# Kernel optimization log

Hardware: AMD Instinct MI355X
Metric: run time of the kernel (lower is better)

## Reference

```python
import jax, jax.numpy as jnp
import numpy as np

TOP_K = 2

def moe_linear(x, router_w, experts_w):
    # x: [T, din]; router_w: [din, E]; experts_w: [E, din, dout]
    T = x.shape[0]
    E = experts_w.shape[0]
    probs = jax.nn.softmax(x @ router_w, axis=-1)            # [T, E]
    topv, topi = jax.lax.top_k(probs, TOP_K)                 # [T, k]
    topv = topv / jnp.sum(topv, axis=-1, keepdims=True)      # renormalize over selected experts
    w = jnp.zeros((T, E), x.dtype).at[jnp.arange(T)[:, None], topi].set(topv)  # dense routing weights
    y = jnp.zeros((T, experts_w.shape[2]), x.dtype)
    for e in range(E):  # small fixed expert loop; avoids [T,E,dout] intermediate
        y = y + w[:, e:e+1] * (x @ experts_w[e])
    return y

def setup_inputs() -> dict:
    key = jax.random.key(0)
    ks = jax.random.split(key, 7)
    B, S, H, I, E = 4, 2048, 1024, 3584, 8
    sH, sI = 1.0 / np.sqrt(H), 1.0 / np.sqrt(I)
    return {
        "hidden_state": jax.random.normal(ks[0], (B, S, H), jnp.float32),
        "gate_router": jax.random.normal(ks[1], (H, E), jnp.float32) * sH,
        "gate_experts": jax.random.normal(ks[2], (E, H, I), jnp.float32) * sH,
        "up_router": jax.random.normal(ks[3], (H, E), jnp.float32) * sH,
        "up_experts": jax.random.normal(ks[4], (E, H, I), jnp.float32) * sH,
        "down_router": jax.random.normal(ks[5], (I, E), jnp.float32) * sI,
        "down_experts": jax.random.normal(ks[6], (E, I, H), jnp.float32) * sI,
    }

def reference(hidden_state, gate_router, gate_experts, up_router, up_experts, down_router, down_experts):
    B, S, H = hidden_state.shape
    x = hidden_state.reshape(B * S, H)
    g = moe_linear(x, gate_router, gate_experts)             # [T, I]
    u = moe_linear(x, up_router, up_experts)                 # [T, I]
    h = jax.nn.silu(g) * u                                   # SwiGLU
    y = moe_linear(h, down_router, down_experts)             # [T, H]
    return y.reshape(B, S, H)
```

## Files before the change

### kernel.cpp

```cpp
#include <hip/hip_runtime.h>
#include <stdint.h>
#include <stdio.h>

#define T_TOK 8192
#define HDIM  1024
#define IDIM  3584
#define NEXP  8
#define NPAIR (T_TOK*2)
#define BM 128
#define BN 128
#define BK 32

typedef float          f32x4 __attribute__((ext_vector_type(4)));
typedef short          s16x8 __attribute__((ext_vector_type(8)));
typedef unsigned short u16x4 __attribute__((ext_vector_type(4)));
typedef unsigned short u16x8 __attribute__((ext_vector_type(8)));

__device__ __forceinline__ unsigned short f2bf_rne(float f) {
  unsigned u = __float_as_uint(f);
  u += 0x7FFFu + ((u >> 16) & 1u);
  return (unsigned short)(u >> 16);
}
__device__ __forceinline__ float bf2f(unsigned short h) {
  return __uint_as_float(((unsigned)h) << 16);
}

__device__ __forceinline__ void gld16(const void* gsrc, void* ldst) {
  typedef const unsigned int __attribute__((address_space(1))) GU;
  typedef unsigned int       __attribute__((address_space(3))) LU;
  __builtin_amdgcn_global_load_lds((GU*)(unsigned long long)gsrc,
                                   (LU*)(unsigned int)(unsigned long long)ldst,
                                   16, 0, 0);
}

__global__ void split_hilo(const float* __restrict__ in,
                           unsigned short* __restrict__ hi,
                           unsigned short* __restrict__ lo, int n4) {
  int i = blockIdx.x*blockDim.x + threadIdx.x;
  int s = gridDim.x*blockDim.x;
  for (; i < n4; i += s) {
    f32x4 v = ((const f32x4*)in)[i];
    u16x4 h, l;
#pragma unroll
    for (int j = 0; j < 4; j++) {
      float f = v[j];
      unsigned short hb = f2bf_rne(f);
      h[j] = hb;
      l[j] = f2bf_rne(f - bf2f(hb));
    }
    ((u16x4*)hi)[i] = h;
    ((u16x4*)lo)[i] = l;
  }
}

__global__ void transpose_split(const float* __restrict__ W,
                                unsigned short* __restrict__ hi,
                                unsigned short* __restrict__ lo,
                                int K, int N) {
  __shared__ float tile[32][33];
  long base = (long)blockIdx.z * K * N;
  int n0 = blockIdx.x*32, k0 = blockIdx.y*32;
  int tx = threadIdx.x, ty = threadIdx.y;
#pragma unroll
  for (int r = 0; r < 4; r++)
    tile[ty+8*r][tx] = W[base + (long)(k0+ty+8*r)*N + n0 + tx];
  __syncthreads();
#pragma unroll
  for (int r = 0; r < 4; r++) {
    float f = tile[tx][ty+8*r];
    long o = base + (long)(n0+ty+8*r)*K + k0 + tx;
    unsigned short hb = f2bf_rne(f);
    hi[o] = hb;
    if (lo) lo[o] = f2bf_rne(f - bf2f(hb));
  }
}

__device__ __forceinline__ void top2_write(const float* acc, int t,
                                           int* __restrict__ topi,
                                           float* __restrict__ topw) {
  int i0 = 0; float l0 = acc[0];
#pragma unroll
  for (int e = 1; e < NEXP; e++) if (acc[e] > l0) { l0 = acc[e]; i0 = e; }
  int i1 = -1; float l1 = -3.4e38f;
#pragma unroll
  for (int e = 0; e < NEXP; e++) if (e != i0 && acc[e] > l1) { l1 = acc[e]; i1 = e; }
  float w0 = 1.f/(1.f + expf(l1 - l0));
  float w1 = 1.f/(1.f + expf(l0 - l1));
  topi[2*t]   = i0; topi[2*t+1] = i1;
  topw[2*t]   = w0; topw[2*t+1] = w1;
}

__global__ __launch_bounds__(256) void router2_topk(
    const float* __restrict__ X,
    const float* __restrict__ RWg, const float* __restrict__ RWu,
    int* __restrict__ tig, float* __restrict__ twg,
    int* __restrict__ tiu, float* __restrict__ twu) {
  int lane = threadIdx.x & 63;
  int t = blockIdx.x*4 + (threadIdx.x>>6);
  const f32x4* xr = (const f32x4*)(X + (long)t*HDIM);
  float ag[NEXP], au[NEXP];
#pragma unroll
  for (int e = 0; e < NEXP; e++) { ag[e] = 0.f; au[e] = 0.f; }
#pragma unroll
  for (int it = 0; it < HDIM/4/64; it++) {
    int c4 = it*64 + lane;
    f32x4 xv = xr[c4];
#pragma unroll
    for (int j = 0; j < 4; j++) {
      const float* wg = RWg + (long)(c4*4+j)*NEXP;
      const float* wu = RWu + (long)(c4*4+j)*NEXP;
#pragma unroll
      for (int e = 0; e < NEXP; e++) { ag[e] += xv[j]*wg[e]; au[e] += xv[j]*wu[e]; }
    }
  }
#pragma unroll
  for (int e = 0; e < NEXP; e++) {
    float vg = ag[e], vu = au[e];
#pragma unroll
    for (int o = 1; o < 64; o <<= 1) { vg += __shfl_xor(vg, o); vu += __shfl_xor(vu, o); }
    ag[e] = vg; au[e] = vu;
  }
  if (lane == 0) { top2_write(ag, t, tig, twg); top2_write(au, t, tiu, twu); }
}

__global__ __launch_bounds__(256) void build_perm(const int* __restrict__ topi,
                                                  const float* __restrict__ topw,
                                                  int* __restrict__ offs,
                                                  int* __restrict__ ptok,
                                                  float* __restrict__ pw) {
  int e = blockIdx.x;
  int tid = threadIdx.x, lane = tid & 63, wv = tid >> 6;
  __shared__ int cnt[NEXP];
  __shared__ int wsum[4];
  if (tid < NEXP) cnt[tid] = 0;
  __syncthreads();
  for (int p = tid; p < NPAIR; p += 256) atomicAdd(&cnt[topi[p]], 1);
  __syncthreads();
  int base = 0;
#pragma unroll
  for (int e2 = 0; e2 < NEXP; e2++) if (e2 < e) base += cnt[e2];
  if (tid == 0) { offs[e] = base; if (e == NEXP-1) offs[NEXP] = base + cnt[e]; }
  for (int p0 = 0; p0 < NPAIR; p0 += 256) {
    int p = p0 + tid;
    bool m = (topi[p] == e);
    unsigned long long b = __ballot(m);
    int lp = __popcll(b & ((1ull << lane) - 1ull));
    if (lane == 0) wsum[wv] = __popcll(b);
    __syncthreads();
    int woff = 0;
#pragma unroll
    for (int w2 = 0; w2 < 4; w2++) if (w2 < wv) woff += wsum[w2];
    int tot = wsum[0] + wsum[1] + wsum[2] + wsum[3];
    if (m) { int dst = base + woff + lp; ptok[dst] = p >> 1; pw[dst] = topw[p]; }
    base += tot;
    __syncthreads();
  }
}

__global__ __launch_bounds__(512) void moe_gemm3_mt(
    const unsigned short* __restrict__ Ahi, const unsigned short* __restrict__ Alo,
    const unsigned short* __restrict__ Bhi, const unsigned short* __restrict__ Blo,
    const int* __restrict__ offs, const int* __restrict__ ptok,
    const float* __restrict__ pw, float* __restrict__ out)
{
  const int e = blockIdx.z;
  const int beg = offs[e];
  const int cnt = offs[e+1] - beg;
  const int m0 = blockIdx.y * 256;
  if (m0 >= cnt) return;
  const int n0 = blockIdx.x * 256;

  __shared__ unsigned short As[2][2][256*32];
  __shared__ unsigned short Bs[2][2][256*32];
  __shared__ int   stok[256];
  __shared__ float swt[256];

  const int tid = threadIdx.x, lane = tid & 63, wv = tid >> 6;
  if (tid < 256) {
    int i = m0 + tid;
    stok[tid] = ptok[beg + (i < cnt ? i : 0)];
    swt[tid]  = (i < cnt) ? pw[beg + i] : 0.f;
  }
  __syncthreads();

  const int srow = lane >> 2;
  const int lc   = ((lane & 3) - ((lane >> 3) & 3)) & 3;
  const long aoff0 = (long)stok[wv*32 +      srow]*HDIM + lc*8;
  const long aoff1 = (long)stok[wv*32 + 16 + srow]*HDIM + lc*8;
  const long boff0 = ((long)e*IDIM + n0 + wv*32 +      srow)*HDIM + lc*8;
  const long boff1 = ((long)e*IDIM + n0 + wv*32 + 16 + srow)*HDIM + lc*8;
  const int dst0 = (wv*32     )*32;
  const int dst1 = (wv*32 + 16)*32;

#define STAGE_A(buf, kk) do {                                   \
    int kl_ = (kk)*32;                                          \
    gld16(Ahi + aoff0 + kl_, &As[buf][0][dst0]);                \
    gld16(Ahi + aoff1 + kl_, &As[buf][0][dst1]);                \
    gld16(Alo + aoff0 + kl_, &As[buf][1][dst0]);                \
    gld16(Alo + aoff1 + kl_, &As[buf][1][dst1]);                \
  } while (0)
#define STAGE_B(buf, kk) do {                                   \
    int kl_ = (kk)*32;                                          \
    gld16(Bhi + boff0 + kl_, &Bs[buf][0][dst0]);                \
    gld16(Bhi + boff1 + kl_, &Bs[buf][0][dst1]);                \
    gld16(Blo + boff0 + kl_, &Bs[buf][1][dst0]);                \
    gld16(Blo + boff1 + kl_, &Bs[buf][1][dst1]);                \
  } while (0)

  const int fl = lane & 15, fg = lane >> 4;
  const int pks = (((fg + (fl >> 1)) & 3) << 3);
  const int wm = wv >> 2, wn = wv & 3;
  const int arow = wm * 128;
  const int bcol = wn * 64;

  f32x4 acc[8][4];
#pragma unroll
  for (int m = 0; m < 8; m++)
#pragma unroll
    for (int n = 0; n < 4; n++) acc[m][n] = {0.f, 0.f, 0.f, 0.f};

  STAGE_A(0, 0);
  STAGE_B(0, 0);
  __syncthreads();

  int cur = 0;
  for (int kt = 0; kt < HDIM/BK; ++kt) {
    const bool st = (kt + 1 < HDIM/BK);
    s16x8 ahf[8], bf4[4];

    if (st) STAGE_A(cur^1, kt + 1);
#pragma unroll
    for (int n = 0; n < 4; n++)
      bf4[n] = *(const s16x8*)&Bs[cur][0][(bcol + n*16 + fl)*32 + pks];
#pragma unroll
    for (int i = 0; i < 8; i++)
      ahf[i] = *(const s16x8*)&As[cur][0][(arow + i*16 + fl)*32 + pks];
    __builtin_amdgcn_s_setprio(1);
#pragma unroll
    for (int i = 0; i < 8; i++)
#pragma unroll
      for (int n = 0; n < 4; n++)
        acc[i][n] = __builtin_amdgcn_mfma_f32_16x16x32_bf16(ahf[i], bf4[n], acc[i][n], 0,0,0);
    __builtin_amdgcn_s_setprio(0);

    if (st) STAGE_B(cur^1, kt + 1);
#pragma unroll
    for (int n = 0; n < 4; n++)
      bf4[n] = *(const s16x8*)&Bs[cur][1][(bcol + n*16 + fl)*32 + pks];
    __builtin_amdgcn_s_setprio(1);
#pragma unroll
    for (int i = 0; i < 8; i++)
#pragma unroll
      for (int n = 0; n < 4; n++)
        acc[i][n] = __builtin_amdgcn_mfma_f32_16x16x32_bf16(ahf[i], bf4[n], acc[i][n], 0,0,0);
    __builtin_amdgcn_s_setprio(0);

#pragma unroll
    for (int i = 0; i < 8; i++)
      ahf[i] = *(const s16x8*)&As[cur][1][(arow + i*16 + fl)*32 + pks];
#pragma unroll
    for (int n = 0; n < 4; n++)
      bf4[n] = *(const s16x8*)&Bs[cur][0][(bcol + n*16 + fl)*32 + pks];
    __builtin_amdgcn_s_setprio(1);
#pragma unroll
    for (int i = 0; i < 8; i++)
#pragma unroll
      for (int n = 0; n < 4; n++)
        acc[i][n] = __builtin_amdgcn_mfma_f32_16x16x32_bf16(ahf[i], bf4[n], acc[i][n], 0,0,0);
    __builtin_amdgcn_s_setprio(0);

    __syncthreads();
    cur ^= 1;
  }
#undef STAGE_A
#undef STAGE_B

#pragma unroll
  for (int m = 0; m < 8; m++)
#pragma unroll
    for (int r = 0; r < 4; r++) {
      int lrow = arow + m*16 + fg*4 + r;
      if (m0 + lrow < cnt) {
        float wt = swt[lrow];
        long ob = (long)stok[lrow]*IDIM + n0 + bcol + fl;
#pragma unroll
        for (int n = 0; n < 4; n++)
          atomicAdd(&out[ob + n*16], wt * acc[m][n][r]);
      }
    }
}

__global__ __launch_bounds__(256) void swiglu_router(
    float* __restrict__ g, const float* __restrict__ u,
    const float* __restrict__ RW,
    int* __restrict__ topi, float* __restrict__ topw) {
  int lane = threadIdx.x & 63;
  int t = blockIdx.x*4 + (threadIdx.x>>6);
  f32x4*       gr = (f32x4*)(g + (long)t*IDIM);
  const f32x4* ur = (const f32x4*)(u + (long)t*IDIM);
  float acc[NEXP];
#pragma unroll
  for (int e = 0; e < NEXP; e++) acc[e] = 0.f;
#pragma unroll
  for (int it = 0; it < IDIM/4/64; it++) {
    int c4 = it*64 + lane;
    f32x4 gv = gr[c4], uv = ur[c4], hv;
#pragma unroll
    for (int j = 0; j < 4; j++) {
      float x = gv[j];
      hv[j] = x * uv[j] / (1.f + expf(-x));
    }
    gr[c4] = hv;
#pragma unroll
    for (int j = 0; j < 4; j++) {
      const float* wr = RW + (long)(c4*4+j)*NEXP;
#pragma unroll
      for (int e = 0; e < NEXP; e++) acc[e] += hv[j]*wr[e];
    }
  }
#pragma unroll
  for (int e = 0; e < NEXP; e++) {
    float v = acc[e];
#pragma unroll
    for (int o = 1; o < 64; o <<= 1) v += __shfl_xor(v, o);
    acc[e] = v;
  }
  if (lane == 0) top2_write(acc, t, topi, topw);
}

__global__ __launch_bounds__(256) void moe_gemm_down(
    const float* __restrict__ Hf, const unsigned short* __restrict__ Bw,
    const int* __restrict__ offs, const int* __restrict__ ptok,
    const float* __restrict__ pw, float* __restrict__ out)
{
  const int K = IDIM, N = HDIM;
  const int e = blockIdx.z;
  const int beg = offs[e];
  const int cnt = offs[e+1] - beg;
  const int m0 = blockIdx.y * BM;
  if (m0 >= cnt) return;
  const int n0 = blockIdx.x * BN;

  __shared__ unsigned short Ah[BM*BK], Bh[BN*BK];
  __shared__ int   stok[BM];
  __shared__ float swt[BM];

  const int tid = threadIdx.x, lane = tid & 63, wv = tid >> 6;
  if (tid < BM) {
    int i = m0 + tid;
    stok[tid] = ptok[beg + (i < cnt ? i : 0)];
    swt[tid]  = (i < cnt) ? pw[beg + i] : 0.f;
  }
  __syncthreads();

  const int arw = tid >> 1, half = tid & 1;
  const float* asrc = Hf + (long)stok[arw]*K + half*16;
  const int awoff = arw*BK + half*16;

  const int srow = lane >> 2, scol = (lane & 3)*8;
  const int r0 = (wv*2+0)*16 + srow, r1 = (wv*2+1)*16 + srow;
  const long b0 = ((long)e*N + n0 + r0)*K + scol;
  const long b1 = ((long)e*N + n0 + r1)*K + scol;
  unsigned short* dB0 = &Bh[(wv*2+0)*16*BK];
  unsigned short* dB1 = &Bh[(wv*2+1)*16*BK];

  f32x4 zero = {0.f,0.f,0.f,0.f};
  f32x4 acc[4][4];
#pragma unroll
  for (int i = 0; i < 4; i++)
#pragma unroll
    for (int j = 0; j < 4; j++) acc[i][j] = zero;

  const int arow = (wv>>1)*64, bcol = (wv&1)*64;
  const int fl = lane & 15, fg = lane >> 4;

  f32x4 p0, p1, p2, p3;
#define LOADA(kk) do {                        \
    p0 = ((const f32x4*)(asrc + (kk)))[0];    \
    p1 = ((const f32x4*)(asrc + (kk)))[1];    \
    p2 = ((const f32x4*)(asrc + (kk)))[2];    \
    p3 = ((const f32x4*)(asrc + (kk)))[3];    \
  } while (0)

  LOADA(0);

  for (int kk = 0; kk < K; kk += BK) {
    __syncthreads();
    gld16(Bw + b0 + kk, dB0);
    gld16(Bw + b1 + kk, dB1);
    u16x8 ha, hb2;
    ha[0]=f2bf_rne(p0[0]); ha[1]=f2bf_rne(p0[1]); ha[2]=f2bf_rne(p0[2]); ha[3]=f2bf_rne(p0[3]);
    ha[4]=f2bf_rne(p1[0]); ha[5]=f2bf_rne(p1[1]); ha[6]=f2bf_rne(p1[2]); ha[7]=f2bf_rne(p1[3]);
    hb2[0]=f2bf_rne(p2[0]); hb2[1]=f2bf_rne(p2[1]); hb2[2]=f2bf_rne(p2[2]); hb2[3]=f2bf_rne(p2[3]);
    hb2[4]=f2bf_rne(p3[0]); hb2[5]=f2bf_rne(p3[1]); hb2[6]=f2bf_rne(p3[2]); hb2[7]=f2bf_rne(p3[3]);
    *(u16x8*)&Ah[awoff]   = ha;
    *(u16x8*)&Ah[awoff+8] = hb2;
    asm volatile("s_waitcnt vmcnt(0)" ::: "memory");
    __syncthreads();

    if (kk + BK < K) LOADA(kk + BK);

    s16x8 ahf[4], bhf[4];
#pragma unroll
    for (int i = 0; i < 4; i++) {
      ahf[i] = *(const s16x8*)&Ah[(arow + i*16 + fl)*BK + fg*8];
      bhf[i] = *(const s16x8*)&Bh[(bcol + i*16 + fl)*BK + fg*8];
    }
#pragma unroll
    for (int i = 0; i < 4; i++)
#pragma unroll
      for (int j = 0; j < 4; j++)
        acc[i][j] = __builtin_amdgcn_mfma_f32_16x16x32_bf16(ahf[i], bhf[j], acc[i][j], 0,0,0);
  }
#undef LOADA

#pragma unroll
  for (int i = 0; i < 4; i++)
#pragma unroll
    for (int r = 0; r < 4; r++) {
      int lrow = arow + i*16 + fg*4 + r;
      if (m0 + lrow < cnt) {
        float wt = swt[lrow];
        long ob = (long)stok[lrow]*N + n0 + bcol + fl;
#pragma unroll
        for (int j = 0; j < 4; j++)
          atomicAdd(&out[ob + j*16], wt * acc[i][j][r]);
      }
    }
}

extern "C" void kernel_launch(void* const* d_in, const int* in_sizes, int n_in,
                              void* d_out, int out_size, void* d_ws, size_t ws_size,
                              hipStream_t stream)
{
  (void)in_sizes; (void)n_in;
  const float* x   = (const float*)d_in[0];
  const float* grt = (const float*)d_in[1];
  const float* gex = (const float*)d_in[2];
  const float* urt = (const float*)d_in[3];
  const float* uex = (const float*)d_in[4];
  const float* drt = (const float*)d_in[5];
  const float* dex = (const float*)d_in[6];
  float* out = (float*)d_out;

  char* base = (char*)d_ws;
  size_t off = 0;
  auto alloc = [&](size_t b) -> void* {
    void* r = base + off;
    off = (off + b + 255) & ~(size_t)255;
    return r;
  };
  const size_t szXH = (size_t)T_TOK*HDIM*2;
  const size_t szW  = (size_t)NEXP*HDIM*IDIM*2;
  const size_t szGI = (size_t)T_TOK*IDIM*4;

  unsigned short* xhi   = (unsigned short*)alloc(szXH);
  unsigned short* xlo   = (unsigned short*)alloc(szXH);
  unsigned short* wg_hi = (unsigned short*)alloc(szW);
  unsigned short* wg_lo = (unsigned short*)alloc(szW);
  unsigned short* wu_hi = (unsigned short*)alloc(szW);
  unsigned short* wu_lo = (unsigned short*)alloc(szW);
  float* gbuf = (float*)alloc(szGI);
  int*   topi_g = (int*)alloc(NPAIR*4);  float* topw_g = (float*)alloc(NPAIR*4);
  int*   topi_u = (int*)alloc(NPAIR*4);  float* topw_u = (float*)alloc(NPAIR*4);
  int*   topi_d = (int*)alloc(NPAIR*4);  float* topw_d = (float*)alloc(NPAIR*4);
  int* offs_g = (int*)alloc(64);
  int* offs_u = (int*)alloc(64);
  int* offs_d = (int*)alloc(64);
  int*   ptok_g = (int*)alloc(NPAIR*4);  float* pw_g = (float*)alloc(NPAIR*4);
  int*   ptok_u = (int*)alloc(NPAIR*4);  float* pw_u = (float*)alloc(NPAIR*4);
  int*   ptok_d = (int*)alloc(NPAIR*4);  float* pw_d = (float*)alloc(NPAIR*4);

  float*          ubuf  = (float*)wg_hi;
  unsigned short* wd_hi = wu_hi;

  if (off > ws_size) {
    fprintf(stderr, "[moe] ws too small: need %zu bytes, have %zu\n", off, ws_size);
    hipMemsetAsync(d_out, 0, (size_t)out_size*sizeof(float), stream);
    return;
  }

  hipMemsetAsync(gbuf, 0, szGI, stream);
  hipMemsetAsync(d_out, 0, (size_t)out_size*sizeof(float), stream);

  split_hilo<<<2048, 256, 0, stream>>>(x, xhi, xlo, T_TOK*HDIM/4);
  transpose_split<<<dim3(IDIM/32, HDIM/32, NEXP), dim3(32,8), 0, stream>>>(gex, wg_hi, wg_lo, HDIM, IDIM);
  transpose_split<<<dim3(IDIM/32, HDIM/32, NEXP), dim3(32,8), 0, stream>>>(uex, wu_hi, wu_lo, HDIM, IDIM);
  router2_topk<<<T_TOK/4, 256, 0, stream>>>(x, grt, urt, topi_g, topw_g, topi_u, topw_u);
  build_perm<<<NEXP, 256, 0, stream>>>(topi_g, topw_g, offs_g, ptok_g, pw_g);
  build_perm<<<NEXP, 256, 0, stream>>>(topi_u, topw_u, offs_u, ptok_u, pw_u);

  moe_gemm3_mt<<<dim3(IDIM/256, 32, NEXP), 512, 0, stream>>>(
      xhi, xlo, wg_hi, wg_lo, offs_g, ptok_g, pw_g, gbuf);

  hipMemsetAsync(ubuf, 0, szGI, stream);
  moe_gemm3_mt<<<dim3(IDIM/256, 32, NEXP), 512, 0, stream>>>(
      xhi, xlo, wu_hi, wu_lo, offs_u, ptok_u, pw_u, ubuf);

  transpose_split<<<dim3(HDIM/32, IDIM/32, NEXP), dim3(32,8), 0, stream>>>(dex, wd_hi, nullptr, IDIM, HDIM);

  swiglu_router<<<T_TOK/4, 256, 0, stream>>>(gbuf, ubuf, drt, topi_d, topw_d);
  build_perm<<<NEXP, 256, 0, stream>>>(topi_d, topw_d, offs_d, ptok_d, pw_d);

  moe_gemm_down<<<dim3(HDIM/BN, T_TOK/BM, NEXP), 256, 0, stream>>>(
      gbuf, wd_hi, offs_d, ptok_d, pw_d, out);
}
```

Measured before the change: 1.732 ms.

## Fuse x split into router, vectorize transposes, bf16 SwiGLU output, pipeline down GEMM

The separate split_hilo pass is folded into the router kernel, so x is read once to produce both the bf16 hi/lo copies and the routing logits. The weight transpose-split kernel now uses 16-byte loads and 8-byte stores. The SwiGLU kernel writes a bf16 activation buffer, and the down GEMM loads it through global_load_lds into double-buffered LDS instead of converting fp32 rows in registers each K step. The up/gate GEMM loads the hi and lo B fragments once per K step instead of reloading them, which raises register pressure in that kernel.

```diff
diff --git a/kernel.cpp b/kernel.cpp
--- a/kernel.cpp
+++ b/kernel.cpp
@@ -7,8 +7,6 @@
 #define IDIM  3584
 #define NEXP  8
 #define NPAIR (T_TOK*2)
-#define BM 128
-#define BN 128
 #define BK 32
 
 typedef float          f32x4 __attribute__((ext_vector_type(4)));
@@ -33,48 +31,6 @@
                                    16, 0, 0);
 }
 
-__global__ void split_hilo(const float* __restrict__ in,
-                           unsigned short* __restrict__ hi,
-                           unsigned short* __restrict__ lo, int n4) {
-  int i = blockIdx.x*blockDim.x + threadIdx.x;
-  int s = gridDim.x*blockDim.x;
-  for (; i < n4; i += s) {
-    f32x4 v = ((const f32x4*)in)[i];
-    u16x4 h, l;
-#pragma unroll
-    for (int j = 0; j < 4; j++) {
-      float f = v[j];
-      unsigned short hb = f2bf_rne(f);
-      h[j] = hb;
-      l[j] = f2bf_rne(f - bf2f(hb));
-    }
-    ((u16x4*)hi)[i] = h;
-    ((u16x4*)lo)[i] = l;
-  }
-}
-
-__global__ void transpose_split(const float* __restrict__ W,
-                                unsigned short* __restrict__ hi,
-                                unsigned short* __restrict__ lo,
-                                int K, int N) {
-  __shared__ float tile[32][33];
-  long base = (long)blockIdx.z * K * N;
-  int n0 = blockIdx.x*32, k0 = blockIdx.y*32;
-  int tx = threadIdx.x, ty = threadIdx.y;
-#pragma unroll
-  for (int r = 0; r < 4; r++)
-    tile[ty+8*r][tx] = W[base + (long)(k0+ty+8*r)*N + n0 + tx];
-  __syncthreads();
-#pragma unroll
-  for (int r = 0; r < 4; r++) {
-    float f = tile[tx][ty+8*r];
-    long o = base + (long)(n0+ty+8*r)*K + k0 + tx;
-    unsigned short hb = f2bf_rne(f);
-    hi[o] = hb;
-    if (lo) lo[o] = f2bf_rne(f - bf2f(hb));
-  }
-}
-
 __device__ __forceinline__ void top2_write(const float* acc, int t,
                                            int* __restrict__ topi,
                                            float* __restrict__ topw) {
@@ -90,14 +46,17 @@
   topw[2*t]   = w0; topw[2*t+1] = w1;
 }
 
-__global__ __launch_bounds__(256) void router2_topk(
+__global__ __launch_bounds__(256) void split_router(
     const float* __restrict__ X,
     const float* __restrict__ RWg, const float* __restrict__ RWu,
+    unsigned short* __restrict__ xhi, unsigned short* __restrict__ xlo,
     int* __restrict__ tig, float* __restrict__ twg,
     int* __restrict__ tiu, float* __restrict__ twu) {
   int lane = threadIdx.x & 63;
   int t = blockIdx.x*4 + (threadIdx.x>>6);
   const f32x4* xr = (const f32x4*)(X + (long)t*HDIM);
+  u16x4* hr = (u16x4*)(xhi + (long)t*HDIM);
+  u16x4* lr = (u16x4*)(xlo + (long)t*HDIM);
   float ag[NEXP], au[NEXP];
 #pragma unroll
   for (int e = 0; e < NEXP; e++) { ag[e] = 0.f; au[e] = 0.f; }
@@ -105,6 +64,14 @@
   for (int it = 0; it < HDIM/4/64; it++) {
     int c4 = it*64 + lane;
     f32x4 xv = xr[c4];
+    u16x4 hh, ll;
+#pragma unroll
+    for (int j = 0; j < 4; j++) {
+      unsigned short hb = f2bf_rne(xv[j]);
+      hh[j] = hb;
+      ll[j] = f2bf_rne(xv[j] - bf2f(hb));
+    }
+    hr[c4] = hh; lr[c4] = ll;
 #pragma unroll
     for (int j = 0; j < 4; j++) {
       const float* wg = RWg + (long)(c4*4+j)*NEXP;
@@ -121,6 +88,33 @@
     ag[e] = vg; au[e] = vu;
   }
   if (lane == 0) { top2_write(ag, t, tig, twg); top2_write(au, t, tiu, twu); }
+}
+
+__global__ void transpose_split_v(const float* __restrict__ W,
+                                  unsigned short* __restrict__ hi,
+                                  unsigned short* __restrict__ lo,
+                                  int K, int N) {
+  __shared__ float t[32][33];
+  long base = (long)blockIdx.z * K * N;
+  int n0 = blockIdx.x*32, k0 = blockIdx.y*32;
+  int id = threadIdx.y*8 + threadIdx.x;
+  int lrr = id >> 3, lcq = id & 7;
+  f32x4 v = *(const f32x4*)&W[base + (long)(k0+lrr)*N + n0 + lcq*4];
+  t[lrr][lcq*4+0] = v[0]; t[lrr][lcq*4+1] = v[1];
+  t[lrr][lcq*4+2] = v[2]; t[lrr][lcq*4+3] = v[3];
+  __syncthreads();
+  int n = threadIdx.y, kq = threadIdx.x;
+  u16x4 h, l;
+#pragma unroll
+  for (int r = 0; r < 4; r++) {
+    float f = t[kq*4+r][n];
+    unsigned short hb = f2bf_rne(f);
+    h[r] = hb;
+    l[r] = f2bf_rne(f - bf2f(hb));
+  }
+  long o = base + (long)(n0+n)*K + k0 + kq*4;
+  *(u16x4*)&hi[o] = h;
+  if (lo) *(u16x4*)&lo[o] = l;
 }
 
 __global__ __launch_bounds__(256) void build_perm(const int* __restrict__ topi,
@@ -226,12 +220,15 @@
   int cur = 0;
   for (int kt = 0; kt < HDIM/BK; ++kt) {
     const bool st = (kt + 1 < HDIM/BK);
-    s16x8 ahf[8], bf4[4];
+    s16x8 ahf[8], bhi4[4], blo4[4];
 
     if (st) STAGE_A(cur^1, kt + 1);
 #pragma unroll
     for (int n = 0; n < 4; n++)
-      bf4[n] = *(const s16x8*)&Bs[cur][0][(bcol + n*16 + fl)*32 + pks];
+      bhi4[n] = *(const s16x8*)&Bs[cur][0][(bcol + n*16 + fl)*32 + pks];
+#pragma unroll
+    for (int n = 0; n < 4; n++)
+      blo4[n] = *(const s16x8*)&Bs[cur][1][(bcol + n*16 + fl)*32 + pks];
 #pragma unroll
     for (int i = 0; i < 8; i++)
       ahf[i] = *(const s16x8*)&As[cur][0][(arow + i*16 + fl)*32 + pks];
@@ -240,33 +237,27 @@
     for (int i = 0; i < 8; i++)
 #pragma unroll
       for (int n = 0; n < 4; n++)
-        acc[i][n] = __builtin_amdgcn_mfma_f32_16x16x32_bf16(ahf[i], bf4[n], acc[i][n], 0,0,0);
+        acc[i][n] = __builtin_amdgcn_mfma_f32_16x16x32_bf16(ahf[i], bhi4[n], acc[i][n], 0,0,0);
     __builtin_amdgcn_s_setprio(0);
 
     if (st) STAGE_B(cur^1, kt + 1);
-#pragma unroll
-    for (int n = 0; n < 4; n++)
-      bf4[n] = *(const s16x8*)&Bs[cur][1][(bcol + n*16 + fl)*32 + pks];
     __builtin_amdgcn_s_setprio(1);
 #pragma unroll
     for (int i = 0; i < 8; i++)
 #pragma unroll
       for (int n = 0; n < 4; n++)
-        acc[i][n] = __builtin_amdgcn_mfma_f32_16x16x32_bf16(ahf[i], bf4[n], acc[i][n], 0,0,0);
+        acc[i][n] = __builtin_amdgcn_mfma_f32_16x16x32_bf16(ahf[i], blo4[n], acc[i][n], 0,0,0);
     __builtin_amdgcn_s_setprio(0);
 
 #pragma unroll
     for (int i = 0; i < 8; i++)
       ahf[i] = *(const s16x8*)&As[cur][1][(arow + i*16 + fl)*32 + pks];
-#pragma unroll
-    for (int n = 0; n < 4; n++)
-      bf4[n] = *(const s16x8*)&Bs[cur][0][(bcol + n*16 + fl)*32 + pks];
     __builtin_amdgcn_s_setprio(1);
 #pragma unroll
     for (int i = 0; i < 8; i++)
 #pragma unroll
       for (int n = 0; n < 4; n++)
-        acc[i][n] = __builtin_amdgcn_mfma_f32_16x16x32_bf16(ahf[i], bf4[n], acc[i][n], 0,0,0);
+        acc[i][n] = __builtin_amdgcn_mfma_f32_16x16x32_bf16(ahf[i], bhi4[n], acc[i][n], 0,0,0);
     __builtin_amdgcn_s_setprio(0);
 
     __syncthreads();
@@ -290,14 +281,16 @@
     }
 }
 
-__global__ __launch_bounds__(256) void swiglu_router(
-    float* __restrict__ g, const float* __restrict__ u,
+__global__ __launch_bounds__(256) void swiglu_router_bf(
+    const float* __restrict__ g, const float* __restrict__ u,
+    unsigned short* __restrict__ hb,
     const float* __restrict__ RW,
     int* __restrict__ topi, float* __restrict__ topw) {
   int lane = threadIdx.x & 63;
   int t = blockIdx.x*4 + (threadIdx.x>>6);
-  f32x4*       gr = (f32x4*)(g + (long)t*IDIM);
+  const f32x4* gr = (const f32x4*)(g + (long)t*IDIM);
   const f32x4* ur = (const f32x4*)(u + (long)t*IDIM);
+  u16x4*       hr = (u16x4*)(hb + (long)t*IDIM);
   float acc[NEXP];
 #pragma unroll
   for (int e = 0; e < NEXP; e++) acc[e] = 0.f;
@@ -305,12 +298,14 @@
   for (int it = 0; it < IDIM/4/64; it++) {
     int c4 = it*64 + lane;
     f32x4 gv = gr[c4], uv = ur[c4], hv;
+    u16x4 hh;
 #pragma unroll
     for (int j = 0; j < 4; j++) {
       float x = gv[j];
       hv[j] = x * uv[j] / (1.f + expf(-x));
-    }
-    gr[c4] = hv;
+      hh[j] = f2bf_rne(hv[j]);
+    }
+    hr[c4] = hh;
 #pragma unroll
     for (int j = 0; j < 4; j++) {
       const float* wr = RW + (long)(c4*4+j)*NEXP;
@@ -328,8 +323,8 @@
   if (lane == 0) top2_write(acc, t, topi, topw);
 }
 
-__global__ __launch_bounds__(256) void moe_gemm_down(
-    const float* __restrict__ Hf, const unsigned short* __restrict__ Bw,
+__global__ __launch_bounds__(256) void moe_gemm_down_bf(
+    const unsigned short* __restrict__ Hb, const unsigned short* __restrict__ Bw,
     const int* __restrict__ offs, const int* __restrict__ ptok,
     const float* __restrict__ pw, float* __restrict__ out)
 {
@@ -337,94 +332,86 @@
   const int e = blockIdx.z;
   const int beg = offs[e];
   const int cnt = offs[e+1] - beg;
-  const int m0 = blockIdx.y * BM;
+  const int m0 = blockIdx.y * 128;
   if (m0 >= cnt) return;
-  const int n0 = blockIdx.x * BN;
-
-  __shared__ unsigned short Ah[BM*BK], Bh[BN*BK];
-  __shared__ int   stok[BM];
-  __shared__ float swt[BM];
+  const int n0 = blockIdx.x * 128;
+
+  __shared__ unsigned short As[2][128*32], Bs[2][128*32];
+  __shared__ int   stok[128];
+  __shared__ float swt[128];
 
   const int tid = threadIdx.x, lane = tid & 63, wv = tid >> 6;
-  if (tid < BM) {
+  if (tid < 128) {
     int i = m0 + tid;
     stok[tid] = ptok[beg + (i < cnt ? i : 0)];
     swt[tid]  = (i < cnt) ? pw[beg + i] : 0.f;
   }
   __syncthreads();
 
-  const int arw = tid >> 1, half = tid & 1;
-  const float* asrc = Hf + (long)stok[arw]*K + half*16;
-  const int awoff = arw*BK + half*16;
-
-  const int srow = lane >> 2, scol = (lane & 3)*8;
-  const int r0 = (wv*2+0)*16 + srow, r1 = (wv*2+1)*16 + srow;
-  const long b0 = ((long)e*N + n0 + r0)*K + scol;
-  const long b1 = ((long)e*N + n0 + r1)*K + scol;
-  unsigned short* dB0 = &Bh[(wv*2+0)*16*BK];
-  unsigned short* dB1 = &Bh[(wv*2+1)*16*BK];
-
-  f32x4 zero = {0.f,0.f,0.f,0.f};
+  const int srow = lane >> 2;
+  const int lc   = ((lane & 3) - ((lane >> 3) & 3)) & 3;
+  const long aoff0 = (long)stok[wv*32 +      srow]*K + lc*8;
+  const long aoff1 = (long)stok[wv*32 + 16 + srow]*K + lc*8;
+  const long boff0 = ((long)e*N + n0 + wv*32 +      srow)*K + lc*8;
+  const long boff1 = ((long)e*N + n0 + wv*32 + 16 + srow)*K + lc*8;
+  const int dst0 = (wv*32     )*32;
+  const int dst1 = (wv*32 + 16)*32;
+
+#define STAGE(buf, kt) do {                                 \
+    int kl_ = (kt)*32;                                      \
+    gld16(Hb + aoff0 + kl_, &As[buf][dst0]);                \
+    gld16(Hb + aoff1 + kl_, &As[buf][dst1]);                \
+    gld16(Bw + boff0 + kl_, &Bs[buf][dst0]);                \
+    gld16(Bw + boff1 + kl_, &Bs[buf][dst1]);                \
+  } while (0)
+
+  const int fl = lane & 15, fg = lane >> 4;
+  const int pks = (((fg + (fl >> 1)) & 3) << 3);
+  const int arow = (wv >> 1)*64, bcol = (wv & 1)*64;
+
   f32x4 acc[4][4];
 #pragma unroll
-  for (int i = 0; i < 4; i++)
-#pragma unroll
-    for (int j = 0; j < 4; j++) acc[i][j] = zero;
-
-  const int arow = (wv>>1)*64, bcol = (wv&1)*64;
-  const int fl = lane & 15, fg = lane >> 4;
-
-  f32x4 p0, p1, p2, p3;
-#define LOADA(kk) do {                        \
-    p0 = ((const f32x4*)(asrc + (kk)))[0];    \
-    p1 = ((const f32x4*)(asrc + (kk)))[1];    \
-    p2 = ((const f32x4*)(asrc + (kk)))[2];    \
-    p3 = ((const f32x4*)(asrc + (kk)))[3];    \
-  } while (0)
-
-  LOADA(0);
-
-  for (int kk = 0; kk < K; kk += BK) {
+  for (int m = 0; m < 4; m++)
+#pragma unroll
+    for (int n = 0; n < 4; n++) acc[m][n] = {0.f, 0.f, 0.f, 0.f};
+
+  STAGE(0, 0);
+  __syncthreads();
+
+  int cur = 0;
+  for (int kt = 0; kt < K/BK; ++kt) {
+    if (kt + 1 < K/BK) STAGE(cur^1, kt + 1);
+
+    s16x8 ahf[4], bhf[4];
+#pragma unroll
+    for (int i = 0; i < 4; i++) {
+      ahf[i] = *(const s16x8*)&As[cur][(arow + i*16 + fl)*32 + pks];
+      bhf[i] = *(const s16x8*)&Bs[cur][(bcol + i*16 + fl)*32 + pks];
+    }
+    __builtin_amdgcn_s_setprio(1);
+#pragma unroll
+    for (int i = 0; i < 4; i++)
+#pragma unroll
+      for (int n = 0; n < 4; n++)
+        acc[i][n] = __builtin_amdgcn_mfma_f32_16x16x32_bf16(ahf[i], bhf[n], acc[i][n], 0,0,0);
+    __builtin_amdgcn_s_setprio(0);
+
     __syncthreads();
-    gld16(Bw + b0 + kk, dB0);
-    gld16(Bw + b1 + kk, dB1);
-    u16x8 ha, hb2;
-    ha[0]=f2bf_rne(p0[0]); ha[1]=f2bf_rne(p0[1]); ha[2]=f2bf_rne(p0[2]); ha[3]=f2bf_rne(p0[3]);
-    ha[4]=f2bf_rne(p1[0]); ha[5]=f2bf_rne(p1[1]); ha[6]=f2bf_rne(p1[2]); ha[7]=f2bf_rne(p1[3]);
-    hb2[0]=f2bf_rne(p2[0]); hb2[1]=f2bf_rne(p2[1]); hb2[2]=f2bf_rne(p2[2]); hb2[3]=f2bf_rne(p2[3]);
-    hb2[4]=f2bf_rne(p3[0]); hb2[5]=f2bf_rne(p3[1]); hb2[6]=f2bf_rne(p3[2]); hb2[7]=f2bf_rne(p3[3]);
-    *(u16x8*)&Ah[awoff]   = ha;
-    *(u16x8*)&Ah[awoff+8] = hb2;
-    asm volatile("s_waitcnt vmcnt(0)" ::: "memory");
-    __syncthreads();
-
-    if (kk + BK < K) LOADA(kk + BK);
-
-    s16x8 ahf[4], bhf[4];
-#pragma unroll
-    for (int i = 0; i < 4; i++) {
-      ahf[i] = *(const s16x8*)&Ah[(arow + i*16 + fl)*BK + fg*8];
-      bhf[i] = *(const s16x8*)&Bh[(bcol + i*16 + fl)*BK + fg*8];
-    }
-#pragma unroll
-    for (int i = 0; i < 4; i++)
-#pragma unroll
-      for (int j = 0; j < 4; j++)
-        acc[i][j] = __builtin_amdgcn_mfma_f32_16x16x32_bf16(ahf[i], bhf[j], acc[i][j], 0,0,0);
-  }
-#undef LOADA
-
-#pragma unroll
-  for (int i = 0; i < 4; i++)
+    cur ^= 1;
+  }
+#undef STAGE
+
+#pragma unroll
+  for (int m = 0; m < 4; m++)
 #pragma unroll
     for (int r = 0; r < 4; r++) {
-      int lrow = arow + i*16 + fg*4 + r;
+      int lrow = arow + m*16 + fg*4 + r;
       if (m0 + lrow < cnt) {
         float wt = swt[lrow];
         long ob = (long)stok[lrow]*N + n0 + bcol + fl;
 #pragma unroll
-        for (int j = 0; j < 4; j++)
-          atomicAdd(&out[ob + j*16], wt * acc[i][j][r]);
+        for (int n = 0; n < 4; n++)
+          atomicAdd(&out[ob + n*16], wt * acc[m][n][r]);
       }
     }
 }
@@ -473,6 +460,7 @@
 
   float*          ubuf  = (float*)wg_hi;
   unsigned short* wd_hi = wu_hi;
+  unsigned short* hbuf  = wu_lo;
 
   if (off > ws_size) {
     fprintf(stderr, "[moe] ws too small: need %zu bytes, have %zu\n", off, ws_size);
@@ -483,10 +471,10 @@
   hipMemsetAsync(gbuf, 0, szGI, stream);
   hipMemsetAsync(d_out, 0, (size_t)out_size*sizeof(float), stream);
 
-  split_hilo<<<2048, 256, 0, stream>>>(x, xhi, xlo, T_TOK*HDIM/4);
-  transpose_split<<<dim3(IDIM/32, HDIM/32, NEXP), dim3(32,8), 0, stream>>>(gex, wg_hi, wg_lo, HDIM, IDIM);
-  transpose_split<<<dim3(IDIM/32, HDIM/32, NEXP), dim3(32,8), 0, stream>>>(uex, wu_hi, wu_lo, HDIM, IDIM);
-  router2_topk<<<T_TOK/4, 256, 0, stream>>>(x, grt, urt, topi_g, topw_g, topi_u, topw_u);
+  split_router<<<T_TOK/4, 256, 0, stream>>>(x, grt, urt, xhi, xlo,
+                                            topi_g, topw_g, topi_u, topw_u);
+  transpose_split_v<<<dim3(IDIM/32, HDIM/32, NEXP), dim3(8,32), 0, stream>>>(gex, wg_hi, wg_lo, HDIM, IDIM);
+  transpose_split_v<<<dim3(IDIM/32, HDIM/32, NEXP), dim3(8,32), 0, stream>>>(uex, wu_hi, wu_lo, HDIM, IDIM);
   build_perm<<<NEXP, 256, 0, stream>>>(topi_g, topw_g, offs_g, ptok_g, pw_g);
   build_perm<<<NEXP, 256, 0, stream>>>(topi_u, topw_u, offs_u, ptok_u, pw_u);
 
@@ -497,11 +485,11 @@
   moe_gemm3_mt<<<dim3(IDIM/256, 32, NEXP), 512, 0, stream>>>(
       xhi, xlo, wu_hi, wu_lo, offs_u, ptok_u, pw_u, ubuf);
 
-  transpose_split<<<dim3(HDIM/32, IDIM/32, NEXP), dim3(32,8), 0, stream>>>(dex, wd_hi, nullptr, IDIM, HDIM);
-
-  swiglu_router<<<T_TOK/4, 256, 0, stream>>>(gbuf, ubuf, drt, topi_d, topw_d);
+  transpose_split_v<<<dim3(HDIM/32, IDIM/32, NEXP), dim3(8,32), 0, stream>>>(dex, wd_hi, nullptr, IDIM, HDIM);
+
+  swiglu_router_bf<<<T_TOK/4, 256, 0, stream>>>(gbuf, ubuf, hbuf, drt, topi_d, topw_d);
   build_perm<<<NEXP, 256, 0, stream>>>(topi_d, topw_d, offs_d, ptok_d, pw_d);
 
-  moe_gemm_down<<<dim3(HDIM/BN, T_TOK/BM, NEXP), 256, 0, stream>>>(
-      gbuf, wd_hi, offs_d, ptok_d, pw_d, out);
-}
+  moe_gemm_down_bf<<<dim3(HDIM/128, 64, NEXP), 256, 0, stream>>>(
+      hbuf, wd_hi, offs_d, ptok_d, pw_d, out);
+}
```

Result: faster. 1.621 ms (-6.4%).
